# Optimization experiments

Hardware: AMD Instinct MI355X
Metric: run time of the kernel (lower is better)

The kernel has to match this reference:

```python
import jax, jax.numpy as jnp
import numpy as np

N_PARTS = 24


def setup_inputs() -> dict:
    key = jax.random.key(0)
    k1, k2, k3, k4 = jax.random.split(key, 4)
    B, C, R = 8, 16, 512
    H = W = 512
    tex = jax.random.normal(k1, (B, C, R, R), dtype=jnp.float32)
    # iuv: channel 0 = part id in [0, 24] (0 == background), channels 1,2 = UV bytes in [0, 255]
    part = jax.random.randint(k2, (B, 1, H, W), 0, N_PARTS + 1, dtype=jnp.int32)
    uv = jax.random.randint(k3, (B, 2, H, W), 0, 256, dtype=jnp.int32)
    iuv = jnp.concatenate([part, uv], axis=1)
    lut = jax.random.uniform(k4, (N_PARTS, 256, 256, 2), dtype=jnp.float32)
    return {"tex": tex, "iuv": iuv, "lut": lut, "tex_res": R}


def reference(tex, iuv, lut, tex_res):
    # tex: [B, C, R, R], iuv: [B, 3, H, W] int, lut: [24, 256, 256, 2]
    B = tex.shape[0]
    mask = iuv[:, 0] > 0                                   # [B, H, W]
    i = jnp.clip(iuv[:, 0] - 1, 0, lut.shape[0] - 1)       # part index, clamped for masked-out pixels
    u = jnp.clip(iuv[:, 1].astype(jnp.float32) / 255.0, 0.0, 1.0)
    v = jnp.clip(iuv[:, 2].astype(jnp.float32) / 255.0, 0.0, 1.0)
    ui = jnp.round(u * 255.0).astype(jnp.int32)
    vi = jnp.round(v * 255.0).astype(jnp.int32)
    uv_smpl = lut[i, vi, ui]                               # [B, H, W, 2]
    u_I = jnp.round(uv_smpl[..., 0] * (tex_res - 1)).astype(jnp.int32)
    v_I = jnp.round((1.0 - uv_smpl[..., 1]) * (tex_res - 1)).astype(jnp.int32)
    b_idx = jnp.arange(B)[:, None, None]                   # [B, 1, 1]
    gathered = tex[b_idx, :, v_I, u_I]                     # [B, H, W, C]
    out = jnp.where(mask[..., None], gathered, jnp.zeros((), tex.dtype))
    return jnp.transpose(out, (0, 3, 1, 2))                # [B, C, H, W]
```

## Files before the change

### kernel.cpp

```cpp
#include <hip/hip_runtime.h>


#define N_PARTS 24

__global__ __launch_bounds__(256) void dp_prep_kernel(
    const float* __restrict__ tex,
    const int*   __restrict__ iuv,
    const float* __restrict__ lut,
    float*       __restrict__ texT,
    int*         __restrict__ offs)
{
    constexpr int C = 16, H = 512, W = 512, R = 512;
    constexpr size_t hw    = (size_t)H * W;
    constexpr size_t plane = (size_t)R * R;
    __shared__ float lds[16 * 516];

    const int bid = blockIdx.x;
    const int g   = bid / 3;
    const int r3  = bid - g * 3;

    if (r3 != 2) {
        const int tid = g * 2 + r3;
        const int b  = tid >> 9;
        const int ty = tid & 511;
        const float* src = tex + (size_t)b * C * plane + (size_t)ty * R;
        const int t = threadIdx.x;

        #pragma unroll
        for (int k = 0; k < 8; ++k) {
            const int f  = k * 256 + t;
            const int c  = f >> 7;
            const int x4 = f & 127;
            const float4 v = *(const float4*)(src + (size_t)c * plane + x4 * 4);
            *(float4*)&lds[c * 516 + x4 * 4] = v;
        }
        __syncthreads();
        float* dst = texT + ((size_t)b * plane + (size_t)ty * R) * C;
        #pragma unroll
        for (int k = 0; k < 8; ++k) {
            const int f  = k * 256 + t;
            const int x  = f >> 2;
            const int c0 = (f & 3) * 4;
            float4 v;
            v.x = lds[(c0 + 0) * 516 + x];
            v.y = lds[(c0 + 1) * 516 + x];
            v.z = lds[(c0 + 2) * 516 + x];
            v.w = lds[(c0 + 3) * 516 + x];
            *(float4*)(dst + (size_t)f * 4) = v;
        }
    } else {
        const float scale = (float)(R - 1);
        const int t = g * 256 + threadIdx.x;
        const int pix4 = t * 4;
        const int b = pix4 >> 18;
        const int p = pix4 & (int)(hw - 1);

        const size_t ibase = (size_t)b * 3 * hw + p;
        const int4 p4 = *(const int4*)(iuv + ibase);
        const int4 u4 = *(const int4*)(iuv + ibase + hw);
        const int4 v4 = *(const int4*)(iuv + ibase + 2 * hw);

        const int parts[4] = {p4.x, p4.y, p4.z, p4.w};
        const int us[4]    = {u4.x, u4.y, u4.z, u4.w};
        const int vs[4]    = {v4.x, v4.y, v4.z, v4.w};

        int4 o4; int* o = &o4.x;
        #pragma unroll
        for (int j = 0; j < 4; ++j) {
            int i = parts[j] - 1;
            i = i < 0 ? 0 : (i > N_PARTS - 1 ? N_PARTS - 1 : i);
            const float fu = fminf(fmaxf((float)us[j] / 255.0f, 0.0f), 1.0f);
            const float fv = fminf(fmaxf((float)vs[j] / 255.0f, 0.0f), 1.0f);
            const int ui = (int)rintf(fu * 255.0f);
            const int vi = (int)rintf(fv * 255.0f);
            const float2 s = *(const float2*)(lut + (((size_t)i * 256 + vi) * 256 + ui) * 2);
            const int uI = (int)rintf(s.x * scale);
            const int vI = (int)rintf((1.0f - s.y) * scale);
            o[j] = (parts[j] > 0) ? (vI * R + uI) : -1;
        }
        *(int4*)(offs + (size_t)b * hw + p) = o4;
    }
}

__global__ __launch_bounds__(256) void dp_gatherT_kernel(
    const float* __restrict__ texT,
    const int*   __restrict__ offs,
    float*       __restrict__ out)
{
    constexpr int C = 16;
    constexpr size_t HW = 512 * 512;
    __shared__ float lds[16 * 256];

    const int b     = blockIdx.x & 7;
    const int inner = blockIdx.x >> 3;
    const int base  = inner * 1024;

    const float* tb   = texT + (size_t)b * HW * C;
    const int*   ob   = offs + (size_t)b * HW + base;
    float*       outb = out  + (size_t)b * C * HW + base;
    const int t = threadIdx.x;

    for (int tile = 0; tile < 4; ++tile) {
        const int p = tile * 256 + t;
        const int o = ob[p];
        const bool m = o >= 0;
        const float4* src = (const float4*)(tb + (size_t)(m ? o : 0) * C);
        float4 r0 = src[0];
        float4 r1 = src[1];
        float4 r2 = src[2];
        float4 r3 = src[3];
        if (!m) {
            r0 = r1 = r2 = r3 = make_float4(0.f, 0.f, 0.f, 0.f);
        }

        if (tile) __syncthreads();
        lds[ 0 * 256 + t] = r0.x;  lds[ 1 * 256 + t] = r0.y;
        lds[ 2 * 256 + t] = r0.z;  lds[ 3 * 256 + t] = r0.w;
        lds[ 4 * 256 + t] = r1.x;  lds[ 5 * 256 + t] = r1.y;
        lds[ 6 * 256 + t] = r1.z;  lds[ 7 * 256 + t] = r1.w;
        lds[ 8 * 256 + t] = r2.x;  lds[ 9 * 256 + t] = r2.y;
        lds[10 * 256 + t] = r2.z;  lds[11 * 256 + t] = r2.w;
        lds[12 * 256 + t] = r3.x;  lds[13 * 256 + t] = r3.y;
        lds[14 * 256 + t] = r3.z;  lds[15 * 256 + t] = r3.w;
        __syncthreads();

        #pragma unroll
        for (int k = 0; k < 4; ++k) {
            const int idx = k * 256 + t;
            const int c   = idx >> 6;
            const int p4  = idx & 63;
            const float4 v = *(const float4*)&lds[c * 256 + p4 * 4];
            *(float4*)(outb + (size_t)c * HW + tile * 256 + p4 * 4) = v;
        }
    }
}

__global__ __launch_bounds__(256) void dp_offsets_kernel(
    const int*   __restrict__ iuv,
    const float* __restrict__ lut,
    int*         __restrict__ offs,
    int R)
{
    constexpr int H = 512, W = 512;
    const float scale = (float)(R - 1);
    const size_t hw = (size_t)H * W;
    const int t = blockIdx.x * blockDim.x + threadIdx.x;
    const int pix4 = t * 4;
    const int b = pix4 >> 18;
    const int p = pix4 & (int)(hw - 1);

    const size_t ibase = (size_t)b * 3 * hw + p;
    const int4 p4 = *(const int4*)(iuv + ibase);
    const int4 u4 = *(const int4*)(iuv + ibase + hw);
    const int4 v4 = *(const int4*)(iuv + ibase + 2 * hw);

    const int parts[4] = {p4.x, p4.y, p4.z, p4.w};
    const int us[4]    = {u4.x, u4.y, u4.z, u4.w};
    const int vs[4]    = {v4.x, v4.y, v4.z, v4.w};

    int4 o4; int* o = &o4.x;
    #pragma unroll
    for (int j = 0; j < 4; ++j) {
        int i = parts[j] - 1;
        i = i < 0 ? 0 : (i > N_PARTS - 1 ? N_PARTS - 1 : i);
        const float fu = fminf(fmaxf((float)us[j] / 255.0f, 0.0f), 1.0f);
        const float fv = fminf(fmaxf((float)vs[j] / 255.0f, 0.0f), 1.0f);
        const int ui = (int)rintf(fu * 255.0f);
        const int vi = (int)rintf(fv * 255.0f);
        const float2 s = *(const float2*)(lut + (((size_t)i * 256 + vi) * 256 + ui) * 2);
        const int uI = (int)rintf(s.x * scale);
        const int vI = (int)rintf((1.0f - s.y) * scale);
        o[j] = (parts[j] > 0) ? (vI * R + uI) : -1;
    }
    *(int4*)(offs + (size_t)b * hw + p) = o4;
}

__global__ __launch_bounds__(256) void dp_gather_kernel(
    const float* __restrict__ tex,
    const int*   __restrict__ offs,
    float*       __restrict__ out,
    int R)
{
    constexpr int C = 16, H = 512, W = 512;
    const size_t hw    = (size_t)H * W;
    const size_t plane = (size_t)R * R;

    const int bid  = blockIdx.x;
    const int xcd  = bid & 7;
    const int slot = bid >> 3;
    const int pl_local = slot >> 8;
    const int inner    = slot & 255;
    const int pidx = xcd * 16 + pl_local;
    const int b = pidx >> 4;
    const int c = pidx & 15;

    const int px = inner * 1024 + threadIdx.x * 4;

    const int4 o4 = *(const int4*)(offs + (size_t)b * hw + px);
    const float* tc = tex + ((size_t)b * C + c) * plane;

    float4 r;
    r.x = (o4.x >= 0) ? tc[o4.x] : 0.0f;
    r.y = (o4.y >= 0) ? tc[o4.y] : 0.0f;
    r.z = (o4.z >= 0) ? tc[o4.z] : 0.0f;
    r.w = (o4.w >= 0) ? tc[o4.w] : 0.0f;

    *(float4*)(out + ((size_t)b * C + c) * hw + px) = r;
}

extern "C" void kernel_launch(void* const* d_in, const int* in_sizes, int n_in,
                              void* d_out, int out_size, void* d_ws, size_t ws_size,
                              hipStream_t stream) {
    const float* tex = (const float*)d_in[0];
    const int*   iuv = (const int*)d_in[1];
    const float* lut = (const float*)d_in[2];
    float*       out = (float*)d_out;

    constexpr int B = 8, C = 16, H = 512, W = 512;
    int R = 512;
    {
        long long pe = (long long)in_sizes[0] / (B * C);
        int r = 1; while ((long long)(r + 1) * (r + 1) <= pe) ++r;
        R = r;
    }

    const size_t texT_bytes = (size_t)B * R * R * C * sizeof(float);
    const size_t offs_bytes = (size_t)B * H * W * sizeof(int);

    if (R == 512 && ws_size >= texT_bytes + offs_bytes) {
        float* texT = (float*)d_ws;
        int*   offs = (int*)((char*)d_ws + texT_bytes);
        dp_prep_kernel<<<dim3(6144), dim3(256), 0, stream>>>(
            tex, iuv, lut, texT, offs);
        dp_gatherT_kernel<<<dim3(2048), dim3(256), 0, stream>>>(
            texT, offs, out);
    } else if (ws_size >= offs_bytes) {
        int* offs = (int*)d_ws;
        dp_offsets_kernel<<<dim3(B * H * W / 4 / 256), dim3(256), 0, stream>>>(
            iuv, lut, offs, R);
        dp_gather_kernel<<<dim3(B * C * (H * W / 1024)), dim3(256), 0, stream>>>(
            tex, offs, out, R);
    }
}
```

Baseline: 344.5 us.

## Fuse offset computation into gather kernel, keep offsets in LDS

Moves the per-pixel LUT lookup and offset computation out of the prep kernel into the gather kernel, storing offsets in shared memory instead of a global buffer. The prep kernel becomes a pure transpose. This removes a global write and re-read of the offset array (8 MB). In exchange, the LUT lookup latency now sits inside the gather kernel before its texture reads can start, and the transpose and offset work no longer run concurrently in one launch.

```diff
diff --git a/kernel.cpp b/kernel.cpp
--- a/kernel.cpp
+++ b/kernel.cpp
@@ -3,62 +3,67 @@
 
 #define N_PARTS 24
 
-__global__ __launch_bounds__(256) void dp_prep_kernel(
+__global__ __launch_bounds__(256) void dp_transpose_kernel(
     const float* __restrict__ tex,
+    float*       __restrict__ texT)
+{
+    constexpr int C = 16, R = 512;
+    constexpr size_t plane = (size_t)R * R;
+    __shared__ float lds[16 * 516];
+
+    const int tid = blockIdx.x;
+    const int b  = tid >> 9;
+    const int ty = tid & 511;
+    const float* src = tex + (size_t)b * C * plane + (size_t)ty * R;
+    const int t = threadIdx.x;
+
+    #pragma unroll
+    for (int k = 0; k < 8; ++k) {
+        const int f  = k * 256 + t;
+        const int c  = f >> 7;
+        const int x4 = f & 127;
+        const float4 v = *(const float4*)(src + (size_t)c * plane + x4 * 4);
+        *(float4*)&lds[c * 516 + x4 * 4] = v;
+    }
+    __syncthreads();
+    float* dst = texT + ((size_t)b * plane + (size_t)ty * R) * C;
+    #pragma unroll
+    for (int k = 0; k < 8; ++k) {
+        const int f  = k * 256 + t;
+        const int x  = f >> 2;
+        const int c0 = (f & 3) * 4;
+        float4 v;
+        v.x = lds[(c0 + 0) * 516 + x];
+        v.y = lds[(c0 + 1) * 516 + x];
+        v.z = lds[(c0 + 2) * 516 + x];
+        v.w = lds[(c0 + 3) * 516 + x];
+        *(float4*)(dst + (size_t)f * 4) = v;
+    }
+}
+
+__global__ __launch_bounds__(256) void dp_gatherT_kernel(
+    const float* __restrict__ texT,
     const int*   __restrict__ iuv,
     const float* __restrict__ lut,
-    float*       __restrict__ texT,
-    int*         __restrict__ offs)
-{
-    constexpr int C = 16, H = 512, W = 512, R = 512;
-    constexpr size_t hw    = (size_t)H * W;
-    constexpr size_t plane = (size_t)R * R;
-    __shared__ float lds[16 * 516];
-
-    const int bid = blockIdx.x;
-    const int g   = bid / 3;
-    const int r3  = bid - g * 3;
-
-    if (r3 != 2) {
-        const int tid = g * 2 + r3;
-        const int b  = tid >> 9;
-        const int ty = tid & 511;
-        const float* src = tex + (size_t)b * C * plane + (size_t)ty * R;
-        const int t = threadIdx.x;
-
-        #pragma unroll
-        for (int k = 0; k < 8; ++k) {
-            const int f  = k * 256 + t;
-            const int c  = f >> 7;
-            const int x4 = f & 127;
-            const float4 v = *(const float4*)(src + (size_t)c * plane + x4 * 4);
-            *(float4*)&lds[c * 516 + x4 * 4] = v;
-        }
-        __syncthreads();
-        float* dst = texT + ((size_t)b * plane + (size_t)ty * R) * C;
-        #pragma unroll
-        for (int k = 0; k < 8; ++k) {
-            const int f  = k * 256 + t;
-            const int x  = f >> 2;
-            const int c0 = (f & 3) * 4;
-            float4 v;
-            v.x = lds[(c0 + 0) * 516 + x];
-            v.y = lds[(c0 + 1) * 516 + x];
-            v.z = lds[(c0 + 2) * 516 + x];
-            v.w = lds[(c0 + 3) * 516 + x];
-            *(float4*)(dst + (size_t)f * 4) = v;
-        }
-    } else {
+    float*       __restrict__ out)
+{
+    constexpr int C = 16, R = 512;
+    constexpr size_t HW = 512 * 512;
+    __shared__ float lds[16 * 256];
+    __shared__ int   offs_lds[1024];
+
+    const int b     = blockIdx.x & 7;
+    const int inner = blockIdx.x >> 3;
+    const int base  = inner * 1024;
+    const int t = threadIdx.x;
+
+    {
         const float scale = (float)(R - 1);
-        const int t = g * 256 + threadIdx.x;
-        const int pix4 = t * 4;
-        const int b = pix4 >> 18;
-        const int p = pix4 & (int)(hw - 1);
-
-        const size_t ibase = (size_t)b * 3 * hw + p;
+        const int pix4 = base + 4 * t;
+        const size_t ibase = (size_t)b * 3 * HW + pix4;
         const int4 p4 = *(const int4*)(iuv + ibase);
-        const int4 u4 = *(const int4*)(iuv + ibase + hw);
-        const int4 v4 = *(const int4*)(iuv + ibase + 2 * hw);
+        const int4 u4 = *(const int4*)(iuv + ibase + HW);
+        const int4 v4 = *(const int4*)(iuv + ibase + 2 * HW);
 
         const int parts[4] = {p4.x, p4.y, p4.z, p4.w};
         const int us[4]    = {u4.x, u4.y, u4.z, u4.w};
@@ -78,31 +83,16 @@
             const int vI = (int)rintf((1.0f - s.y) * scale);
             o[j] = (parts[j] > 0) ? (vI * R + uI) : -1;
         }
-        *(int4*)(offs + (size_t)b * hw + p) = o4;
-    }
-}
-
-__global__ __launch_bounds__(256) void dp_gatherT_kernel(
-    const float* __restrict__ texT,
-    const int*   __restrict__ offs,
-    float*       __restrict__ out)
-{
-    constexpr int C = 16;
-    constexpr size_t HW = 512 * 512;
-    __shared__ float lds[16 * 256];
-
-    const int b     = blockIdx.x & 7;
-    const int inner = blockIdx.x >> 3;
-    const int base  = inner * 1024;
+        *(int4*)&offs_lds[4 * t] = o4;
+    }
+    __syncthreads();
 
     const float* tb   = texT + (size_t)b * HW * C;
-    const int*   ob   = offs + (size_t)b * HW + base;
     float*       outb = out  + (size_t)b * C * HW + base;
-    const int t = threadIdx.x;
 
     for (int tile = 0; tile < 4; ++tile) {
         const int p = tile * 256 + t;
-        const int o = ob[p];
+        const int o = offs_lds[p];
         const bool m = o >= 0;
         const float4* src = (const float4*)(tb + (size_t)(m ? o : 0) * C);
         float4 r0 = src[0];
@@ -227,13 +217,11 @@
     const size_t texT_bytes = (size_t)B * R * R * C * sizeof(float);
     const size_t offs_bytes = (size_t)B * H * W * sizeof(int);
 
-    if (R == 512 && ws_size >= texT_bytes + offs_bytes) {
+    if (R == 512 && ws_size >= texT_bytes) {
         float* texT = (float*)d_ws;
-        int*   offs = (int*)((char*)d_ws + texT_bytes);
-        dp_prep_kernel<<<dim3(6144), dim3(256), 0, stream>>>(
-            tex, iuv, lut, texT, offs);
+        dp_transpose_kernel<<<dim3(4096), dim3(256), 0, stream>>>(tex, texT);
         dp_gatherT_kernel<<<dim3(2048), dim3(256), 0, stream>>>(
-            texT, offs, out);
+            texT, iuv, lut, out);
     } else if (ws_size >= offs_bytes) {
         int* offs = (int*)d_ws;
         dp_offsets_kernel<<<dim3(B * H * W / 4 / 256), dim3(256), 0, stream>>>(
```

Measured after the change: 349.7 us. No clear change (+1.5%).
